# Optimization experiments

Hardware: AMD Instinct MI355X
Metric: run time of the kernel (lower is better)

Reference implementation:

```python
import jax, jax.numpy as jnp
import numpy as np

N = 1024      # number of atoms
L = 64        # latent_size
VOCAB = 20    # vocab_size (len(ATOM_CATEGORIES))


def _lin(key, fan_in, fan_out):
    # mimic torch nn.Linear init: U(-1/sqrt(fan_in), 1/sqrt(fan_in))
    kw, kb = jax.random.split(key)
    s = 1.0 / np.sqrt(fan_in)
    W = jax.random.uniform(kw, (fan_in, fan_out), minval=-s, maxval=s, dtype=jnp.float32)
    b = jax.random.uniform(kb, (fan_out,), minval=-s, maxval=s, dtype=jnp.float32)
    return W, b


def setup_inputs() -> dict:
    key = jax.random.key(0)
    ks = jax.random.split(key, 9)
    We1, be1 = _lin(ks[3], 2 * L + 1, L)   # mlp_e layer 1
    We2, be2 = _lin(ks[4], L, L)           # mlp_e layer 2
    Wh1, bh1 = _lin(ks[5], L + 1, L)       # mlp_h layer 1
    Wh2, bh2 = _lin(ks[6], L, L)           # mlp_h layer 2
    Wo, bo = _lin(ks[7], L, 1)             # output_mlp
    return {
        "atom_categories": jax.random.randint(ks[0], (N,), 0, VOCAB),
        "atom_coordinates": jax.random.normal(ks[1], (N, 3), dtype=jnp.float32),
        "learnable_matrix": jax.random.normal(ks[2], (VOCAB, L), dtype=jnp.float32),
        "We1": We1, "be1": be1, "We2": We2, "be2": be2,
        "Wh1": Wh1, "bh1": bh1, "Wh2": Wh2, "bh2": bh2,
        "Wo": Wo, "bo": bo,
    }


def reference(atom_categories, atom_coordinates, learnable_matrix,
              We1, be1, We2, be2, Wh1, bh1, Wh2, bh2, Wo, bo):
    Z = atom_coordinates
    # init_H: learnable_matrix.T @ one_hot(cat) == row gather
    H = learnable_matrix[atom_categories]                       # [N, L]

    # pairwise squared distances ||Z_i - Z_j||^2
    d2 = jnp.sum((Z[:, None, :] - Z[None, :, :]) ** 2, axis=-1)  # [N, N]

    # mlp_e layer 1 on concat(H_i, H_j, d2): split We1 to avoid materializing concat
    W1i, W1j, w1z = We1[:L], We1[L:2 * L], We1[2 * L]            # [L,L],[L,L],[L]
    pre_i = H @ W1i                                              # [N, L]
    pre_j = H @ W1j                                              # [N, L]
    h1 = jnp.tanh(pre_i[:, None, :] + pre_j[None, :, :]
                  + d2[:, :, None] * w1z + be1)                  # [N, N, L]
    W_e = jnp.tanh(h1 @ We2 + be2)                               # [N, N, L]

    # V[i] = sum over j != i of sum_l W_e[i,j,l]
    total = jnp.sum(W_e, axis=(1, 2))                            # [N]
    diag = jnp.einsum('iil->i', W_e)                             # [N]
    V = total - diag                                             # [N]

    # mlp_h on concat(H_i, V_i): split Wh1
    hh = jnp.tanh(H @ Wh1[:L] + V[:, None] * Wh1[L] + bh1)       # [N, L]
    newH = jnp.tanh(hh @ Wh2 + bh2)                              # [N, L]

    Hsum = jnp.sum(newH, axis=0)                                 # [L]
    return (Hsum @ Wo + bo)[0]                                   # scalar
```

## Files before the change

kernel.cpp:

```cpp
#include <hip/hip_runtime.h>
#include <hip/hip_bf16.h>


#define N_ATOMS 1024
#define L_DIM 64
#define TPB 512
#define CSCALE 2.8853900817779268f

typedef _Float16 f16x8 __attribute__((ext_vector_type(8)));
typedef __fp16  fp16x2 __attribute__((ext_vector_type(2)));
typedef float f32x4 __attribute__((ext_vector_type(4)));

__device__ __forceinline__ float tanh_fast(float x) {
    float e = __builtin_amdgcn_exp2f(x * CSCALE);
    float r = __builtin_amdgcn_rcpf(e + 1.0f);
    return fmaf(-2.0f, r, 1.0f);
}

__global__ __launch_bounds__(256) void k_prep(const int* __restrict__ cat,
                                              const float* __restrict__ LM,
                                              const float* __restrict__ We1,
                                              const float* __restrict__ be1,
                                              float* __restrict__ H,
                                              float* __restrict__ preI,
                                              float* __restrict__ P3,
                                              float* __restrict__ out) {
    int t = threadIdx.x;
    int sub = t >> 6, l = t & 63;
    if (blockIdx.x == 0 && t == 0) out[0] = 0.f;

    __shared__ float W1s[2 * L_DIM * L_DIM];
    __shared__ float hs[4][L_DIM];
#pragma unroll
    for (int p = 0; p < 2 * L_DIM * L_DIM / 256; p++)
        W1s[p * 256 + t] = We1[p * 256 + t];

    float bl = be1[l];

    for (int g = 0; g < 4; g++) {
        int i = blockIdx.x * 16 + g * 4 + sub;
        __syncthreads();
        float hv = LM[cat[i] * L_DIM + l];
        hs[sub][l] = hv;
        H[i * L_DIM + l] = hv;
        __syncthreads();
        float s1 = 0.f, s2 = 0.f;
#pragma unroll
        for (int m = 0; m < L_DIM; m++) {
            float h = hs[sub][m];
            s1 = fmaf(h, W1s[m * L_DIM + l], s1);
            s2 = fmaf(h, W1s[(L_DIM + m) * L_DIM + l], s2);
        }
        preI[i * L_DIM + l] = s1 * CSCALE;
        int cc = i >> 4;
        int Ll = i & 15;
        int quad = (l >> 3) & 3;
        int L = quad * 16 + Ll;
        int gg = ((l >> 5) << 1) | ((l >> 2) & 1);
        int e2 = l & 3;
        P3[cc * 1024 + gg * 256 + L * 4 + e2] = (s2 + bl) * CSCALE;
    }
}

__global__ __launch_bounds__(TPB) void k_main(const float* __restrict__ Z,
                                              const float* __restrict__ We1,
                                              const float* __restrict__ We2,
                                              const float* __restrict__ be2,
                                              const float* __restrict__ preI,
                                              const float* __restrict__ P3,
                                              const float* __restrict__ H,
                                              const float* __restrict__ Wh1,
                                              const float* __restrict__ bh1,
                                              const float* __restrict__ Wh2,
                                              const float* __restrict__ bh2,
                                              const float* __restrict__ Wo,
                                              const float* __restrict__ bo,
                                              float* __restrict__ out) {
    int i = blockIdx.x;
    int t = threadIdx.x;
    int lane = t & 63;
    int wave = t >> 6;
    int nlo = lane & 15;
    int quad = lane >> 4;

    __shared__ float d2s[N_ATOMS];
    __shared__ float red[TPB];
    __shared__ float hrow_s[L_DIM];
    __shared__ float hh_s[L_DIM];
    __shared__ float dgt[L_DIM];
    __shared__ f16x8 bLs[8 * 64];

    float zi0 = Z[i * 3], zi1 = Z[i * 3 + 1], zi2 = Z[i * 3 + 2];
    for (int p = t; p < N_ATOMS; p += TPB) {
        float a = zi0 - Z[p * 3], b = zi1 - Z[p * 3 + 1], c = zi2 - Z[p * 3 + 2];
        d2s[p] = a * a + b * b + c * c;
    }

    f32x4 aiR[4], wzR[4];
#pragma unroll
    for (int g = 0; g < 4; g++) {
        int mb = ((g >> 1) << 5) + (quad << 3) + ((g & 1) << 2);
        aiR[g] = *(const f32x4*)(preI + i * L_DIM + mb);
        f32x4 wz = *(const f32x4*)(We1 + 2 * L_DIM * L_DIM + mb);
        wzR[g] = wz * CSCALE;
    }

    f16x8 bH[4][2];
    float biasR[4];
#pragma unroll
    for (int nt = 0; nt < 4; nt++) {
        float psum = 0.f;
#pragma unroll
        for (int kt = 0; kt < 2; kt++) {
            f16x8 hi8, lo8;
#pragma unroll
            for (int e = 0; e < 8; e++) {
                float x = We2[(kt * 32 + quad * 8 + e) * L_DIM + nt * 16 + nlo];
                psum += x;
                float wp = -2.0f * CSCALE * x;
                _Float16 hi = (_Float16)wp;
                hi8[e] = hi;
                lo8[e] = (_Float16)(wp - (float)hi);
            }
            bH[nt][kt] = hi8;
            if (wave == 0) bLs[(kt * 4 + nt) * 64 + lane] = lo8;
        }
        psum += __shfl_xor(psum, 16);
        psum += __shfl_xor(psum, 32);
        biasR[nt] = CSCALE * (be2[nt * 16 + nlo] + psum);
    }

    const float* Pbase = P3 + wave * 8 * 1024 + lane * 4;
    f32x4 p0 = *(const f32x4*)(Pbase + 0 * 256);
    f32x4 p1 = *(const f32x4*)(Pbase + 1 * 256);
    f32x4 p2 = *(const f32x4*)(Pbase + 2 * 256);
    f32x4 p3 = *(const f32x4*)(Pbase + 3 * 256);

    __syncthreads();

    float Vr = 0.f;
    for (int k = 0; k < 8; k++) {
        int j0 = (wave * 8 + k) * 16;
        float d2 = d2s[j0 + nlo];

        float h[4][4];
#pragma unroll
        for (int e2 = 0; e2 < 4; e2++) {
            {
                float z = fmaf(d2, wzR[0][e2], aiR[0][e2] + p0[e2]);
                h[0][e2] = __builtin_amdgcn_rcpf(__builtin_amdgcn_exp2f(z) + 1.0f);
            }
            {
                float z = fmaf(d2, wzR[1][e2], aiR[1][e2] + p1[e2]);
                h[1][e2] = __builtin_amdgcn_rcpf(__builtin_amdgcn_exp2f(z) + 1.0f);
            }
            {
                float z = fmaf(d2, wzR[2][e2], aiR[2][e2] + p2[e2]);
                h[2][e2] = __builtin_amdgcn_rcpf(__builtin_amdgcn_exp2f(z) + 1.0f);
            }
            {
                float z = fmaf(d2, wzR[3][e2], aiR[3][e2] + p3[e2]);
                h[3][e2] = __builtin_amdgcn_rcpf(__builtin_amdgcn_exp2f(z) + 1.0f);
            }
        }
        union { f16x8 v; fp16x2 h2[4]; } u0, u1;
        u0.h2[0] = __builtin_amdgcn_cvt_pkrtz(h[0][0], h[0][1]);
        u0.h2[1] = __builtin_amdgcn_cvt_pkrtz(h[0][2], h[0][3]);
        u0.h2[2] = __builtin_amdgcn_cvt_pkrtz(h[1][0], h[1][1]);
        u0.h2[3] = __builtin_amdgcn_cvt_pkrtz(h[1][2], h[1][3]);
        u1.h2[0] = __builtin_amdgcn_cvt_pkrtz(h[2][0], h[2][1]);
        u1.h2[1] = __builtin_amdgcn_cvt_pkrtz(h[2][2], h[2][3]);
        u1.h2[2] = __builtin_amdgcn_cvt_pkrtz(h[3][0], h[3][1]);
        u1.h2[3] = __builtin_amdgcn_cvt_pkrtz(h[3][2], h[3][3]);
        f16x8 aH0 = u0.v, aH1 = u1.v;

        if (k < 7) {
            const float* nb = Pbase + (k + 1) * 1024;
            p0 = *(const f32x4*)(nb + 0 * 256);
            p1 = *(const f32x4*)(nb + 1 * 256);
            p2 = *(const f32x4*)(nb + 2 * 256);
            p3 = *(const f32x4*)(nb + 3 * 256);
        }

#pragma unroll
        for (int nt = 0; nt < 4; nt++) {
            f16x8 bl0 = bLs[(0 * 4 + nt) * 64 + lane];
            f16x8 bl1 = bLs[(1 * 4 + nt) * 64 + lane];
            f32x4 acc = {biasR[nt], biasR[nt], biasR[nt], biasR[nt]};
            acc = __builtin_amdgcn_mfma_f32_16x16x32_f16(aH0, bH[nt][0], acc, 0, 0, 0);
            acc = __builtin_amdgcn_mfma_f32_16x16x32_f16(aH0, bl0, acc, 0, 0, 0);
            acc = __builtin_amdgcn_mfma_f32_16x16x32_f16(aH1, bH[nt][1], acc, 0, 0, 0);
            acc = __builtin_amdgcn_mfma_f32_16x16x32_f16(aH1, bl1, acc, 0, 0, 0);
#pragma unroll
            for (int r4 = 0; r4 < 4; r4++) {
                float e = __builtin_amdgcn_exp2f(acc[r4]);
                Vr += __builtin_amdgcn_rcpf(e + 1.0f);
            }
        }
    }

    red[t] = Vr;
    __syncthreads();

    float Rall;
    if (t < 64) {
        float r = 0.f;
#pragma unroll
        for (int w = 0; w < 8; w++) r += red[t + w * 64];
#pragma unroll
        for (int o = 32; o > 0; o >>= 1) r += __shfl_xor(r, o);
        Rall = r;
        int cc = i >> 4, Ll = i & 15;
        int q2 = (t >> 3) & 3;
        int g = ((t >> 5) << 1) | ((t >> 2) & 1);
        float z = preI[i * L_DIM + t] + P3[cc * 1024 + g * 256 + (q2 * 16 + Ll) * 4 + (t & 3)];
        float rr = __builtin_amdgcn_rcpf(__builtin_amdgcn_exp2f(z) + 1.0f);
        dgt[t] = fmaf(-2.0f, rr, 1.0f);
        hrow_s[t] = H[i * L_DIM + t];
    }
    __syncthreads();
    if (t < 64) {
        float S = be2[t];
#pragma unroll
        for (int m = 0; m < L_DIM; m++) S = fmaf(dgt[m], We2[m * L_DIM + t], S);
        float rd = __builtin_amdgcn_rcpf(__builtin_amdgcn_exp2f(S * CSCALE) + 1.0f);
#pragma unroll
        for (int o = 32; o > 0; o >>= 1) rd += __shfl_xor(rd, o);
        float V = fmaf(-2.0f, Rall - rd, (float)(1023 * L_DIM));
        float s = 0.f;
#pragma unroll
        for (int m = 0; m < L_DIM; m++) s = fmaf(hrow_s[m], Wh1[m * L_DIM + t], s);
        s = fmaf(V, Wh1[L_DIM * L_DIM + t], s) + bh1[t];
        hh_s[t] = tanh_fast(s);
    }
    __syncthreads();
    if (t < 64) {
        float s2 = 0.f;
#pragma unroll
        for (int m = 0; m < L_DIM; m++) s2 = fmaf(hh_s[m], Wh2[m * L_DIM + t], s2);
        float nh = tanh_fast(s2 + bh2[t]);
        float w = nh * Wo[t];
#pragma unroll
        for (int o = 32; o > 0; o >>= 1) w += __shfl_down(w, o);
        if (t == 0) atomicAdd(out, w + (i == 0 ? bo[0] : 0.f));
    }
}

extern "C" void kernel_launch(void* const* d_in, const int* in_sizes, int n_in,
                              void* d_out, int out_size, void* d_ws, size_t ws_size,
                              hipStream_t stream) {
    const int*   cat = (const int*)  d_in[0];
    const float* Z   = (const float*)d_in[1];
    const float* LM  = (const float*)d_in[2];
    const float* We1 = (const float*)d_in[3];
    const float* be1 = (const float*)d_in[4];
    const float* We2 = (const float*)d_in[5];
    const float* be2 = (const float*)d_in[6];
    const float* Wh1 = (const float*)d_in[7];
    const float* bh1 = (const float*)d_in[8];
    const float* Wh2 = (const float*)d_in[9];
    const float* bh2 = (const float*)d_in[10];
    const float* Wo  = (const float*)d_in[11];
    const float* bo  = (const float*)d_in[12];
    float* out = (float*)d_out;

    float* ws   = (float*)d_ws;
    float* H    = ws;
    float* preI = H    + N_ATOMS * L_DIM;
    float* P3   = preI + N_ATOMS * L_DIM;

    k_prep<<<N_ATOMS / 16, 256, 0, stream>>>(cat, LM, We1, be1, H, preI, P3, out);
    k_main<<<N_ATOMS, TPB, 0, stream>>>(Z, We1, We2, be2, preI, P3, H,
                                        Wh1, bh1, Wh2, bh2, Wo, bo, out);
}
```

Measured before the change: 137.8 us.

## Split pair kernel into half-row blocks and move node MLP to separate kernel

The main kernel now runs two 256-thread blocks per atom, each covering half of the j range, and writes a partial edge sum to workspace. The serial 64-thread node-MLP tail (diagonal correction, mlp_h, output reduction) moves into a new k_post kernel that handles four atoms per block. This is meant to shorten the idle tail where most threads of a large block waited on single-wave work, and to give finer-grained blocks. In exchange it adds a third kernel launch, duplicates the per-block We2 split setup across twice as many blocks, and adds a global round trip for the partial sums.

```diff
diff --git a/kernel.cpp b/kernel.cpp
--- a/kernel.cpp
+++ b/kernel.cpp
@@ -4,7 +4,7 @@
 
 #define N_ATOMS 1024
 #define L_DIM 64
-#define TPB 512
+#define TPB 256
 #define CSCALE 2.8853900817779268f
 
 typedef _Float16 f16x8 __attribute__((ext_vector_type(8)));
@@ -68,32 +68,25 @@
                                               const float* __restrict__ be2,
                                               const float* __restrict__ preI,
                                               const float* __restrict__ P3,
-                                              const float* __restrict__ H,
-                                              const float* __restrict__ Wh1,
-                                              const float* __restrict__ bh1,
-                                              const float* __restrict__ Wh2,
-                                              const float* __restrict__ bh2,
-                                              const float* __restrict__ Wo,
-                                              const float* __restrict__ bo,
-                                              float* __restrict__ out) {
-    int i = blockIdx.x;
+                                              float* __restrict__ Vpart) {
+    int b = blockIdx.x;
+    int i = b >> 1;
+    int half = b & 1;
     int t = threadIdx.x;
     int lane = t & 63;
     int wave = t >> 6;
     int nlo = lane & 15;
     int quad = lane >> 4;
 
-    __shared__ float d2s[N_ATOMS];
+    __shared__ float d2s[512];
     __shared__ float red[TPB];
-    __shared__ float hrow_s[L_DIM];
-    __shared__ float hh_s[L_DIM];
-    __shared__ float dgt[L_DIM];
     __shared__ f16x8 bLs[8 * 64];
 
     float zi0 = Z[i * 3], zi1 = Z[i * 3 + 1], zi2 = Z[i * 3 + 2];
-    for (int p = t; p < N_ATOMS; p += TPB) {
-        float a = zi0 - Z[p * 3], b = zi1 - Z[p * 3 + 1], c = zi2 - Z[p * 3 + 2];
-        d2s[p] = a * a + b * b + c * c;
+    for (int p = t; p < 512; p += TPB) {
+        int j = half * 512 + p;
+        float a = zi0 - Z[j * 3], bb = zi1 - Z[j * 3 + 1], c = zi2 - Z[j * 3 + 2];
+        d2s[p] = a * a + bb * bb + c * c;
     }
 
     f32x4 aiR[4], wzR[4];
@@ -130,7 +123,7 @@
         biasR[nt] = CSCALE * (be2[nt * 16 + nlo] + psum);
     }
 
-    const float* Pbase = P3 + wave * 8 * 1024 + lane * 4;
+    const float* Pbase = P3 + (half * 32 + wave * 8) * 1024 + lane * 4;
     f32x4 p0 = *(const f32x4*)(Pbase + 0 * 256);
     f32x4 p1 = *(const f32x4*)(Pbase + 1 * 256);
     f32x4 p2 = *(const f32x4*)(Pbase + 2 * 256);
@@ -140,8 +133,8 @@
 
     float Vr = 0.f;
     for (int k = 0; k < 8; k++) {
-        int j0 = (wave * 8 + k) * 16;
-        float d2 = d2s[j0 + nlo];
+        int jl0 = (wave * 8 + k) * 16;
+        float d2 = d2s[jl0 + nlo];
 
         float h[4][4];
 #pragma unroll
@@ -201,49 +194,68 @@
 
     red[t] = Vr;
     __syncthreads();
-
-    float Rall;
     if (t < 64) {
-        float r = 0.f;
-#pragma unroll
-        for (int w = 0; w < 8; w++) r += red[t + w * 64];
+        float r = red[t] + red[t + 64] + red[t + 128] + red[t + 192];
 #pragma unroll
         for (int o = 32; o > 0; o >>= 1) r += __shfl_xor(r, o);
-        Rall = r;
-        int cc = i >> 4, Ll = i & 15;
-        int q2 = (t >> 3) & 3;
-        int g = ((t >> 5) << 1) | ((t >> 2) & 1);
-        float z = preI[i * L_DIM + t] + P3[cc * 1024 + g * 256 + (q2 * 16 + Ll) * 4 + (t & 3)];
-        float rr = __builtin_amdgcn_rcpf(__builtin_amdgcn_exp2f(z) + 1.0f);
-        dgt[t] = fmaf(-2.0f, rr, 1.0f);
-        hrow_s[t] = H[i * L_DIM + t];
-    }
-    __syncthreads();
-    if (t < 64) {
-        float S = be2[t];
-#pragma unroll
-        for (int m = 0; m < L_DIM; m++) S = fmaf(dgt[m], We2[m * L_DIM + t], S);
-        float rd = __builtin_amdgcn_rcpf(__builtin_amdgcn_exp2f(S * CSCALE) + 1.0f);
-#pragma unroll
-        for (int o = 32; o > 0; o >>= 1) rd += __shfl_xor(rd, o);
-        float V = fmaf(-2.0f, Rall - rd, (float)(1023 * L_DIM));
-        float s = 0.f;
-#pragma unroll
-        for (int m = 0; m < L_DIM; m++) s = fmaf(hrow_s[m], Wh1[m * L_DIM + t], s);
-        s = fmaf(V, Wh1[L_DIM * L_DIM + t], s) + bh1[t];
-        hh_s[t] = tanh_fast(s);
-    }
-    __syncthreads();
-    if (t < 64) {
-        float s2 = 0.f;
-#pragma unroll
-        for (int m = 0; m < L_DIM; m++) s2 = fmaf(hh_s[m], Wh2[m * L_DIM + t], s2);
-        float nh = tanh_fast(s2 + bh2[t]);
-        float w = nh * Wo[t];
-#pragma unroll
-        for (int o = 32; o > 0; o >>= 1) w += __shfl_down(w, o);
-        if (t == 0) atomicAdd(out, w + (i == 0 ? bo[0] : 0.f));
-    }
+        if (t == 0) Vpart[b] = r;
+    }
+}
+
+__global__ __launch_bounds__(256) void k_post(const float* __restrict__ Vpart,
+                                              const float* __restrict__ preI,
+                                              const float* __restrict__ P3,
+                                              const float* __restrict__ We2,
+                                              const float* __restrict__ be2,
+                                              const float* __restrict__ H,
+                                              const float* __restrict__ Wh1,
+                                              const float* __restrict__ bh1,
+                                              const float* __restrict__ Wh2,
+                                              const float* __restrict__ bh2,
+                                              const float* __restrict__ Wo,
+                                              const float* __restrict__ bo,
+                                              float* __restrict__ out) {
+    int t = threadIdx.x;
+    int sub = t >> 6, l = t & 63;
+    int i = blockIdx.x * 4 + sub;
+    __shared__ float hrow[4][L_DIM];
+    __shared__ float hh[4][L_DIM];
+    __shared__ float dgt[4][L_DIM];
+
+    int cc = i >> 4, Ll = i & 15;
+    int q2 = (l >> 3) & 3;
+    int g = ((l >> 5) << 1) | ((l >> 2) & 1);
+    float z = preI[i * L_DIM + l] + P3[cc * 1024 + g * 256 + (q2 * 16 + Ll) * 4 + (l & 3)];
+    float rr = __builtin_amdgcn_rcpf(__builtin_amdgcn_exp2f(z) + 1.0f);
+    dgt[sub][l] = fmaf(-2.0f, rr, 1.0f);
+    hrow[sub][l] = H[i * L_DIM + l];
+    __syncthreads();
+
+    float S = be2[l];
+#pragma unroll
+    for (int m = 0; m < L_DIM; m++) S = fmaf(dgt[sub][m], We2[m * L_DIM + l], S);
+    float rd = __builtin_amdgcn_rcpf(__builtin_amdgcn_exp2f(S * CSCALE) + 1.0f);
+#pragma unroll
+    for (int o = 32; o > 0; o >>= 1) rd += __shfl_xor(rd, o);
+
+    float Rall = Vpart[2 * i] + Vpart[2 * i + 1];
+    float V = fmaf(-2.0f, Rall - rd, (float)(1023 * L_DIM));
+
+    float s = 0.f;
+#pragma unroll
+    for (int m = 0; m < L_DIM; m++) s = fmaf(hrow[sub][m], Wh1[m * L_DIM + l], s);
+    s = fmaf(V, Wh1[L_DIM * L_DIM + l], s) + bh1[l];
+    hh[sub][l] = tanh_fast(s);
+    __syncthreads();
+
+    float s2 = 0.f;
+#pragma unroll
+    for (int m = 0; m < L_DIM; m++) s2 = fmaf(hh[sub][m], Wh2[m * L_DIM + l], s2);
+    float nh = tanh_fast(s2 + bh2[l]);
+    float w = nh * Wo[l];
+#pragma unroll
+    for (int o = 32; o > 0; o >>= 1) w += __shfl_down(w, o);
+    if (l == 0) atomicAdd(out, w + (i == 0 ? bo[0] : 0.f));
 }
 
 extern "C" void kernel_launch(void* const* d_in, const int* in_sizes, int n_in,
@@ -264,12 +276,14 @@
     const float* bo  = (const float*)d_in[12];
     float* out = (float*)d_out;
 
-    float* ws   = (float*)d_ws;
-    float* H    = ws;
-    float* preI = H    + N_ATOMS * L_DIM;
-    float* P3   = preI + N_ATOMS * L_DIM;
+    float* ws    = (float*)d_ws;
+    float* H     = ws;
+    float* preI  = H     + N_ATOMS * L_DIM;
+    float* P3    = preI  + N_ATOMS * L_DIM;
+    float* Vpart = P3    + N_ATOMS * L_DIM;
 
     k_prep<<<N_ATOMS / 16, 256, 0, stream>>>(cat, LM, We1, be1, H, preI, P3, out);
-    k_main<<<N_ATOMS, TPB, 0, stream>>>(Z, We1, We2, be2, preI, P3, H,
-                                        Wh1, bh1, Wh2, bh2, Wo, bo, out);
-}
+    k_main<<<2 * N_ATOMS, TPB, 0, stream>>>(Z, We1, We2, be2, preI, P3, Vpart);
+    k_post<<<N_ATOMS / 4, 256, 0, stream>>>(Vpart, preI, P3, We2, be2, H,
+                                            Wh1, bh1, Wh2, bh2, Wo, bo, out);
+}
```

Result: slower. 148.4 us (+7.7%).
